# Optimization experiments

Measured on AMD Instinct MI355X. Metric: run time of the kernel, lower is better.

Reference implementation:

```python
import jax, jax.numpy as jnp
import numpy as np
import math

B, S, D = 2, 8192, 1024
NW, SHIFT = 16, 256          # num_windows, shift_window
NH, DH = 16, 64              # heads = D // dim_head
DFF = 4 * D
EPS = 1e-6


def setup_inputs() -> dict:
    key = jax.random.key(0)
    ks = jax.random.split(key, 12)
    s = 1.0 / math.sqrt(D)
    return {
        "x": jax.random.normal(ks[0], (B, S, D), jnp.float32),
        "wq": jax.random.normal(ks[1], (D, NH * DH), jnp.float32) * s,
        "wk": jax.random.normal(ks[2], (D, NH * DH), jnp.float32) * s,
        "wv": jax.random.normal(ks[3], (D, NH * DH), jnp.float32) * s,
        "wo": jax.random.normal(ks[4], (NH * DH, D), jnp.float32) * s,
        "g_attn": jnp.ones((D,), jnp.float32),
        "g_ff": jnp.ones((D,), jnp.float32),
        "w1": jax.random.normal(ks[5], (D, DFF), jnp.float32) * s,
        "b1": jnp.zeros((DFF,), jnp.float32),
        "w2": jax.random.normal(ks[6], (DFF, D), jnp.float32) * (1.0 / math.sqrt(DFF)),
        "b2": jnp.zeros((D,), jnp.float32),
    }


def _rmsnorm(x, g):
    return x * g * jax.lax.rsqrt(jnp.mean(x * x, axis=-1, keepdims=True) + EPS)


def reference(x, wq, wk, wv, wo, g_attn, g_ff, w1, b1, w2, b2):
    skip = x
    h = _rmsnorm(x, g_attn)
    # shift (note: source rolls by -shift both before AND after attention)
    h = jnp.roll(h, -SHIFT, axis=1)
    # window partition: [B, NW, n, D]
    n = S // NW
    h = h.reshape(B, NW, n, D)
    q = (h @ wq).reshape(B, NW, n, NH, DH)
    k = (h @ wk).reshape(B, NW, n, NH, DH)
    v = (h @ wv).reshape(B, NW, n, NH, DH)
    scores = jnp.einsum('bwqhd,bwkhd->bwhqk', q, k) * (1.0 / math.sqrt(DH))
    a = jax.nn.softmax(scores, axis=-1)
    o = jnp.einsum('bwhqk,bwkhd->bwqhd', a, v).reshape(B, NW, n, NH * DH)
    o = (o @ wo).reshape(B, S, D)
    o = jnp.roll(o, -SHIFT, axis=1)  # faithful to source (rolls -shift again)
    x = o + skip
    skip = x
    h = _rmsnorm(x, g_ff)
    h = jax.nn.gelu(h @ w1 + b1) @ w2 + b2
    return h + skip
```

## Files before the change

### kernel.cpp

```cpp
#include <hip/hip_runtime.h>
#include <stdint.h>

#define S_LEN 8192
#define D_DIM 1024
#define SHIFT_W 256
#define NROWS 16384

typedef __bf16 bf16;
typedef __bf16 bf16x8 __attribute__((ext_vector_type(8)));
typedef __bf16 bf16x4 __attribute__((ext_vector_type(4)));
typedef float f32x4 __attribute__((ext_vector_type(4)));

typedef __attribute__((address_space(1))) const void gas_t;
typedef __attribute__((address_space(3))) void las_t;

__device__ __forceinline__ void load_lds16(const void* g, void* l) {
  __builtin_amdgcn_global_load_lds((gas_t*)g, (las_t*)l, 16, 0, 0);
}

__device__ __forceinline__ int xcd_swizzle(int orig, int nwg) {
  return (orig & 7) * (nwg >> 3) + (orig >> 3);
}

__global__ __launch_bounds__(256) void k_transpose_cvt(const float* __restrict__ in,
                                                       bf16* __restrict__ out,
                                                       int R, int C) {
  __shared__ float tile[32][33];
  int lx = threadIdx.x & 31, ly = threadIdx.x >> 5;
  int tc = blockIdx.x * 32, tr = blockIdx.y * 32;
#pragma unroll
  for (int i = 0; i < 4; i++)
    tile[ly + i * 8][lx] = in[(size_t)(tr + ly + i * 8) * C + tc + lx];
  __syncthreads();
#pragma unroll
  for (int i = 0; i < 4; i++)
    out[(size_t)(tc + ly + i * 8) * R + tr + lx] = (bf16)tile[lx][ly + i * 8];
}

__global__ __launch_bounds__(256) void k_rmsnorm(const float* __restrict__ x,
                                                 const float* __restrict__ g,
                                                 bf16* __restrict__ out, int shift) {
  int row = blockIdx.x;
  int b = row >> 13, r = row & (S_LEN - 1);
  int src = (b << 13) | ((r + shift) & (S_LEN - 1));
  int t = threadIdx.x;
  float4 v = *(const float4*)(x + (size_t)src * D_DIM + t * 4);
  float ss = v.x * v.x + v.y * v.y + v.z * v.z + v.w * v.w;
#pragma unroll
  for (int off = 32; off; off >>= 1) ss += __shfl_xor(ss, off);
  __shared__ float red[4];
  if ((t & 63) == 0) red[t >> 6] = ss;
  __syncthreads();
  ss = red[0] + red[1] + red[2] + red[3];
  float sc = rsqrtf(ss * (1.0f / D_DIM) + 1e-6f);
  float4 gv = *(const float4*)(g + t * 4);
  bf16x4 o;
  o[0] = (bf16)(v.x * gv.x * sc);
  o[1] = (bf16)(v.y * gv.y * sc);
  o[2] = (bf16)(v.z * gv.z * sc);
  o[3] = (bf16)(v.w * gv.w * sc);
  *(bf16x4*)(out + (size_t)row * D_DIM + t * 4) = o;
}

#define VM8 asm volatile("s_waitcnt vmcnt(8)" ::: "memory")
#define VM4 asm volatile("s_waitcnt vmcnt(4)" ::: "memory")
#define VM0 asm volatile("s_waitcnt vmcnt(0)" ::: "memory")
#define BAR __builtin_amdgcn_s_barrier()

#define STAGE(kbase, kk, dbuf)                                        \
  {                                                                   \
    const bf16* _ga = gAs + (kbase) + (kk) * 32;                      \
    const bf16* _gb = gBs + (kbase) + (kk) * 32;                      \
    char* _lb = smem + (dbuf) * 65536 + (kk) * 16384 + wv * 1024;     \
    load_lds16(_ga, _lb);                                             \
    load_lds16(_ga + 128 * (size_t)K, _lb + 8192);                    \
    load_lds16(_gb, _lb + 32768);                                     \
    load_lds16(_gb + 128 * (size_t)K, _lb + 40960);                   \
  }

#define DS_A(mh, kkof)                                                \
  {                                                                   \
    _Pragma("unroll") for (int mf = 0; mf < 4; mf++)                  \
        a[mf] = *(const bf16x8*)(Ac + (kkof) + aBase + (mh) * 4096 + mf * 1024); \
  }
#define DS_B(kkof)                                                    \
  {                                                                   \
    _Pragma("unroll") for (int nf = 0; nf < 4; nf++)                  \
        bfr[nf] = *(const bf16x8*)(Ac + (kkof) + bBase + nf * 1024);  \
  }
#define MFMA16(mh)                                                    \
  {                                                                   \
    __builtin_amdgcn_s_setprio(1);                                    \
    _Pragma("unroll") for (int mf = 0; mf < 4; mf++)                  \
        _Pragma("unroll") for (int nf = 0; nf < 4; nf++)              \
            acc[(mh) * 4 + mf][nf] = __builtin_amdgcn_mfma_f32_16x16x32_bf16( \
                a[mf], bfr[nf], acc[(mh) * 4 + mf][nf], 0, 0, 0);     \
    __builtin_amdgcn_s_setprio(0);                                    \
  }

template <int EPI>
__global__ __launch_bounds__(512, 2) void k_gemm(const bf16* __restrict__ A,
                                                 const bf16* __restrict__ BT,
                                                 bf16* __restrict__ obf,
                                                 float* __restrict__ of32,
                                                 const float* __restrict__ bias,
                                                 const float* __restrict__ skip,
                                                 int K, int ldc) {
  extern __shared__ char smem[];
  const int tid = threadIdx.x;
  const int wv = tid >> 6, lane = tid & 63;
  const int lr = lane & 15, lg = lane >> 4;
  const int wm = wv >> 2, wn = wv & 3;

  const int NB = gridDim.x >> 6;
  const int xcd = blockIdx.x & 7;
  const int l = blockIdx.x >> 3;
  const int mb = ((xcd & 3) << 4) + (l & 15);
  const int nb = (xcd >> 2) * (NB >> 1) + (l >> 4);
  const int m0 = mb * 256, n0 = nb * 256;

  const int sr = ((tid >> 6) << 4) + ((tid >> 2) & 15);
  const int skoff = (((tid & 3) ^ ((tid >> 3) & 3)) << 3);
  const bf16* gAs = A + (size_t)(m0 + sr) * K + skoff;
  const bf16* gBs = BT + (size_t)(n0 + sr) * K + skoff;

  const int kchunk = (lg ^ ((lr >> 1) & 3)) << 4;
  const int aBase = wm * 8192 + lr * 64 + kchunk;
  const int bBase = 32768 + wn * 4096 + lr * 64 + kchunk;

  f32x4 acc[8][4] = {};
  const int nt = K >> 6;

  STAGE(0, 0, 0);
  STAGE(0, 1, 0);
  STAGE(64, 0, 1);
  VM8;
  BAR;

  int cur = 0;
  for (int t = 0; t < nt; ++t) {
    const int k0 = t << 6;
    const char* Ac = smem + cur * 65536;
    bf16x8 a[4], bfr[4];
    DS_A(0, 0);
    DS_B(0);
    BAR;
    if (t + 1 < nt) STAGE(k0 + 64, 1, cur ^ 1);
    MFMA16(0);
    DS_A(1, 0);
    BAR;
    MFMA16(1);
    if (t + 1 < nt) { VM8; } else { VM0; }
    BAR;
    DS_A(0, 16384);
    DS_B(16384);
    BAR;
    if (t + 2 < nt) STAGE(k0 + 128, 0, cur);
    MFMA16(0);
    DS_A(1, 16384);
    BAR;
    MFMA16(1);
    if (t + 1 < nt) {
      if (t + 2 < nt) { VM8; } else { VM4; }
      BAR;
    }
    cur ^= 1;
  }

  float* lds_f = (float*)smem;
  const int erow = tid >> 3;
  const int ecol0 = (tid & 7) * 4;
#pragma unroll
  for (int mh = 0; mh < 2; mh++)
#pragma unroll
    for (int wmr = 0; wmr < 2; wmr++) {
      BAR;
      if (wm == wmr) {
#pragma unroll
        for (int mf = 0; mf < 4; mf++) {
          int lrow = mf * 16 + lg * 4;
#pragma unroll
          for (int nf = 0; nf < 4; nf++) {
            int lcol = wn * 64 + nf * 16 + lr;
#pragma unroll
            for (int ii = 0; ii < 4; ii++)
              lds_f[(lrow + ii) * 260 + lcol] = acc[mh * 4 + mf][nf][ii];
          }
        }
      }
      BAR;
      int gr = m0 + wmr * 128 + mh * 64 + erow;
      size_t orow;
      if constexpr (EPI == 1) {
        int b = gr >> 13, rr = gr & (S_LEN - 1);
        orow = (size_t)((b << 13) | ((rr - SHIFT_W) & (S_LEN - 1))) * ldc;
      } else {
        orow = (size_t)gr * ldc;
      }
#pragma unroll
      for (int j = 0; j < 8; j++) {
        f32x4 v = *(const f32x4*)&lds_f[erow * 260 + ecol0 + j * 32];
        int col = n0 + ecol0 + j * 32;
        if constexpr (EPI == 0) {
          bf16x4 o;
#pragma unroll
          for (int e = 0; e < 4; e++) o[e] = (bf16)v[e];
          *(bf16x4*)(obf + orow + col) = o;
        } else if constexpr (EPI == 1) {
          f32x4 s = *(const f32x4*)(skip + orow + col);
          f32x4 r = v + s;
          *(f32x4*)(of32 + orow + col) = r;
        } else if constexpr (EPI == 2) {
          f32x4 bi = *(const f32x4*)(bias + col);
          bf16x4 o;
#pragma unroll
          for (int e = 0; e < 4; e++) {
            float z = v[e] + bi[e];
            float u = 0.7978845608f * (z + 0.044715f * z * z * z);
            u = fminf(fmaxf(u, -15.f), 15.f);
            float ex = __expf(2.f * u);
            o[e] = (bf16)(0.5f * z * (1.f + (ex - 1.f) / (ex + 1.f)));
          }
          *(bf16x4*)(obf + orow + col) = o;
        } else {
          f32x4 bi = *(const f32x4*)(bias + col);
          f32x4 s = *(const f32x4*)(skip + orow + col);
          f32x4 r = v + bi + s;
          *(f32x4*)(of32 + orow + col) = r;
        }
      }
    }
}

__global__ __launch_bounds__(256) void k_attn(const bf16* __restrict__ qkv,
                                              bf16* __restrict__ out) {
  __shared__ __align__(16) char Qs[8192];
  __shared__ __align__(16) char Ks[8192];
  __shared__ __align__(16) char Vs[8192];
  __shared__ __align__(16) char Ps[4][2048];
  const int tid = threadIdx.x;
  const int wave = tid >> 6, lane = tid & 63;
  const int lr = lane & 15, lg = lane >> 4;
  const int bid = xcd_swizzle(blockIdx.x, gridDim.x);
  const int qt = bid & 7;
  const int h = (bid >> 3) & 15;
  const int bw = bid >> 7;
  const int rowbase = bw * 512;
  const int qrow0 = rowbase + qt * 64;

  {
    int r = tid >> 2, c0 = tid & 3;
    const bf16* src = qkv + (size_t)(qrow0 + r) * 3072 + h * 64;
#pragma unroll
    for (int j = 0; j < 2; j++) {
      int ch = c0 + j * 4;
      uint4 val = *(const uint4*)(src + ch * 8);
      int byte = (r * 128 + ch * 16) ^ ((r & 7) << 4);
      *(uint4*)(Qs + byte) = val;
    }
  }
  __syncthreads();
  bf16x8 qf[2];
  {
    int qr = wave * 16 + lr;
#pragma unroll
    for (int kk = 0; kk < 2; kk++) {
      int byte = (qr * 128 + (kk * 32 + lg * 8) * 2) ^ ((qr & 7) << 4);
      qf[kk] = *(const bf16x8*)(Qs + byte);
    }
  }

  f32x4 oacc[4] = {};
  float m_run = -__builtin_inff(), l_run = 0.f;

  for (int kt = 0; kt < 8; ++kt) {
    __syncthreads();
    {
      int r = tid >> 2, c0 = tid & 3;
      const bf16* ksrc = qkv + (size_t)(rowbase + kt * 64 + r) * 3072 + 1024 + h * 64;
      const bf16* vsrc = ksrc + 1024;
#pragma unroll
      for (int j = 0; j < 2; j++) {
        int ch = c0 + j * 4;
        uint4 val = *(const uint4*)(ksrc + ch * 8);
        int byte = (r * 128 + ch * 16) ^ ((r & 7) << 4);
        *(uint4*)(Ks + byte) = val;
      }
#pragma unroll
      for (int j = 0; j < 2; j++) {
        int ch = c0 + j * 4;
        bf16x8 vv = *(const bf16x8*)(vsrc + ch * 8);
#pragma unroll
        for (int e = 0; e < 8; e++) {
          int d = ch * 8 + e;
          int byte = (d * 128 + r * 2) ^ ((d & 7) << 4);
          *(bf16*)(Vs + byte) = vv[e];
        }
      }
    }
    __syncthreads();
    f32x4 sc[4] = {};
#pragma unroll
    for (int kk = 0; kk < 2; kk++)
#pragma unroll
      for (int mf = 0; mf < 4; mf++) {
        int kr = mf * 16 + lr;
        int byte = (kr * 128 + (kk * 32 + lg * 8) * 2) ^ ((kr & 7) << 4);
        bf16x8 kf = *(const bf16x8*)(Ks + byte);
        sc[mf] = __builtin_amdgcn_mfma_f32_16x16x32_bf16(kf, qf[kk], sc[mf], 0, 0, 0);
      }
    float mx = -__builtin_inff();
#pragma unroll
    for (int mf = 0; mf < 4; mf++)
#pragma unroll
      for (int i = 0; i < 4; i++) mx = fmaxf(mx, sc[mf][i]);
    mx = fmaxf(mx, __shfl_xor(mx, 16));
    mx = fmaxf(mx, __shfl_xor(mx, 32));
    float mnew = fmaxf(m_run, mx);
    float alpha = __expf(0.125f * (m_run - mnew));
    float lsum = 0.f;
    float ps[4][4];
#pragma unroll
    for (int mf = 0; mf < 4; mf++)
#pragma unroll
      for (int i = 0; i < 4; i++) {
        float p = __expf(0.125f * (sc[mf][i] - mnew));
        ps[mf][i] = p;
        lsum += p;
      }
    lsum += __shfl_xor(lsum, 16);
    lsum += __shfl_xor(lsum, 32);
    l_run = l_run * alpha + lsum;
    m_run = mnew;
#pragma unroll
    for (int dm = 0; dm < 4; dm++) oacc[dm] *= alpha;
#pragma unroll
    for (int mf = 0; mf < 4; mf++) {
      bf16x4 pv;
#pragma unroll
      for (int i = 0; i < 4; i++) pv[i] = (bf16)ps[mf][i];
      int byte = (lr * 128 + (mf * 16 + lg * 4) * 2) ^ ((lr & 7) << 4);
      *(bf16x4*)(Ps[wave] + byte) = pv;
    }
#pragma unroll
    for (int kk = 0; kk < 2; kk++) {
      int pbyte = (lr * 128 + (kk * 32 + lg * 8) * 2) ^ ((lr & 7) << 4);
      bf16x8 pf = *(const bf16x8*)(Ps[wave] + pbyte);
#pragma unroll
      for (int dm = 0; dm < 4; dm++) {
        int d = dm * 16 + lr;
        int byte = (d * 128 + (kk * 32 + lg * 8) * 2) ^ ((d & 7) << 4);
        bf16x8 vf = *(const bf16x8*)(Vs + byte);
        oacc[dm] = __builtin_amdgcn_mfma_f32_16x16x32_bf16(vf, pf, oacc[dm], 0, 0, 0);
      }
    }
  }
  float inv = 1.f / l_run;
  int rowq = qrow0 + wave * 16 + lr;
#pragma unroll
  for (int dm = 0; dm < 4; dm++) {
    bf16x4 ov;
#pragma unroll
    for (int i = 0; i < 4; i++) ov[i] = (bf16)(oacc[dm][i] * inv);
    *(bf16x4*)(out + (size_t)rowq * 1024 + h * 64 + dm * 16 + lg * 4) = ov;
  }
}

extern "C" void kernel_launch(void* const* d_in, const int* in_sizes, int n_in,
                              void* d_out, int out_size, void* d_ws, size_t ws_size,
                              hipStream_t stream) {
  const float* x = (const float*)d_in[0];
  const float* wq = (const float*)d_in[1];
  const float* wk = (const float*)d_in[2];
  const float* wv = (const float*)d_in[3];
  const float* wo = (const float*)d_in[4];
  const float* ga = (const float*)d_in[5];
  const float* gf = (const float*)d_in[6];
  const float* w1 = (const float*)d_in[7];
  const float* b1 = (const float*)d_in[8];
  const float* w2 = (const float*)d_in[9];
  const float* b2 = (const float*)d_in[10];
  float* out = (float*)d_out;

  char* ws = (char*)d_ws;
  const size_t MB = 1024 * 1024;
  bf16* wqkvT = (bf16*)(ws);
  bf16* woT = (bf16*)(ws + 6 * MB);
  bf16* w1T = (bf16*)(ws + 8 * MB);
  bf16* w2T = (bf16*)(ws + 16 * MB);
  float* x1 = (float*)(ws + 24 * MB);
  bf16* hbuf = (bf16*)(ws + 88 * MB);
  bf16* qkv = (bf16*)(ws + 120 * MB);
  bf16* mid = qkv;

  (void)hipFuncSetAttribute(reinterpret_cast<const void*>(&k_gemm<0>),
                            hipFuncAttributeMaxDynamicSharedMemorySize, 131072);
  (void)hipFuncSetAttribute(reinterpret_cast<const void*>(&k_gemm<1>),
                            hipFuncAttributeMaxDynamicSharedMemorySize, 131072);
  (void)hipFuncSetAttribute(reinterpret_cast<const void*>(&k_gemm<2>),
                            hipFuncAttributeMaxDynamicSharedMemorySize, 131072);
  (void)hipFuncSetAttribute(reinterpret_cast<const void*>(&k_gemm<3>),
                            hipFuncAttributeMaxDynamicSharedMemorySize, 131072);

  k_transpose_cvt<<<dim3(32, 32), 256, 0, stream>>>(wq, wqkvT, 1024, 1024);
  k_transpose_cvt<<<dim3(32, 32), 256, 0, stream>>>(wk, wqkvT + 1024 * 1024, 1024, 1024);
  k_transpose_cvt<<<dim3(32, 32), 256, 0, stream>>>(wv, wqkvT + 2 * 1024 * 1024, 1024, 1024);
  k_transpose_cvt<<<dim3(32, 32), 256, 0, stream>>>(wo, woT, 1024, 1024);
  k_transpose_cvt<<<dim3(128, 32), 256, 0, stream>>>(w1, w1T, 1024, 4096);
  k_transpose_cvt<<<dim3(32, 128), 256, 0, stream>>>(w2, w2T, 4096, 1024);

  k_rmsnorm<<<NROWS, 256, 0, stream>>>(x, ga, hbuf, SHIFT_W);
  k_gemm<0><<<64 * 12, 512, 131072, stream>>>(hbuf, wqkvT, qkv, nullptr, nullptr, nullptr, 1024, 3072);
  k_attn<<<4096, 256, 0, stream>>>(qkv, hbuf);
  k_gemm<1><<<64 * 4, 512, 131072, stream>>>(hbuf, woT, nullptr, x1, nullptr, x, 1024, 1024);
  k_rmsnorm<<<NROWS, 256, 0, stream>>>(x1, gf, hbuf, 0);
  k_gemm<2><<<64 * 16, 512, 131072, stream>>>(hbuf, w1T, mid, nullptr, b1, nullptr, 1024, 4096);
  k_gemm<3><<<64 * 4, 512, 131072, stream>>>(mid, w2T, nullptr, out, b2, x1, 4096, 1024);
}
```

Before: 666.1 us.

## Double-buffer LDS fragment registers to overlap ds_reads with MFMA in GEMM

Restructures the GEMM main loop to use two sets of A and B register fragments, so each shared-memory fragment read for the next MFMA batch is issued before the current batch runs. The next tile's first fragments are prefetched at the end of each iteration, and the vmcnt waits and barriers are reordered. The aim is to hide LDS read latency behind matrix instructions. The cost is more vector registers, which could cause spills or lower occupancy at launch bounds of 512 threads with 2 blocks. The new wait and barrier ordering also risks a race between global-to-LDS staging and the fragment reads.

Result: no change. 659.8 us (-0.9%).

```diff
diff --git a/kernel.cpp b/kernel.cpp
--- a/kernel.cpp
+++ b/kernel.cpp
@@ -62,7 +62,6 @@
   *(bf16x4*)(out + (size_t)row * D_DIM + t * 4) = o;
 }
 
-#define VM8 asm volatile("s_waitcnt vmcnt(8)" ::: "memory")
 #define VM4 asm volatile("s_waitcnt vmcnt(4)" ::: "memory")
 #define VM0 asm volatile("s_waitcnt vmcnt(0)" ::: "memory")
 #define BAR __builtin_amdgcn_s_barrier()
@@ -78,23 +77,23 @@
     load_lds16(_gb + 128 * (size_t)K, _lb + 40960);                   \
   }
 
-#define DS_A(mh, kkof)                                                \
+#define LOAD_A(dst, mh, kkof, base)                                   \
   {                                                                   \
     _Pragma("unroll") for (int mf = 0; mf < 4; mf++)                  \
-        a[mf] = *(const bf16x8*)(Ac + (kkof) + aBase + (mh) * 4096 + mf * 1024); \
-  }
-#define DS_B(kkof)                                                    \
+        dst[mf] = *(const bf16x8*)((base) + (kkof) + aBase + (mh) * 4096 + mf * 1024); \
+  }
+#define LOAD_B(dst, kkof, base)                                       \
   {                                                                   \
     _Pragma("unroll") for (int nf = 0; nf < 4; nf++)                  \
-        bfr[nf] = *(const bf16x8*)(Ac + (kkof) + bBase + nf * 1024);  \
-  }
-#define MFMA16(mh)                                                    \
+        dst[nf] = *(const bf16x8*)((base) + (kkof) + bBase + nf * 1024); \
+  }
+#define MFMA16(mh, A_, B_)                                            \
   {                                                                   \
     __builtin_amdgcn_s_setprio(1);                                    \
     _Pragma("unroll") for (int mf = 0; mf < 4; mf++)                  \
         _Pragma("unroll") for (int nf = 0; nf < 4; nf++)              \
             acc[(mh) * 4 + mf][nf] = __builtin_amdgcn_mfma_f32_16x16x32_bf16( \
-                a[mf], bfr[nf], acc[(mh) * 4 + mf][nf], 0, 0, 0);     \
+                A_[mf], B_[nf], acc[(mh) * 4 + mf][nf], 0, 0, 0);     \
     __builtin_amdgcn_s_setprio(0);                                    \
   }
 
@@ -131,40 +130,45 @@
   f32x4 acc[8][4] = {};
   const int nt = K >> 6;
 
+  bf16x8 aX[4], aY[4], b0[4], b1[4];
+
   STAGE(0, 0, 0);
   STAGE(0, 1, 0);
-  STAGE(64, 0, 1);
-  VM8;
+  if (nt > 1) STAGE(64, 0, 1);
+  VM4;
   BAR;
-
-  int cur = 0;
+  LOAD_A(aX, 0, 0, smem);
+  LOAD_B(b0, 0, smem);
+
   for (int t = 0; t < nt; ++t) {
-    const int k0 = t << 6;
-    const char* Ac = smem + cur * 65536;
-    bf16x8 a[4], bfr[4];
-    DS_A(0, 0);
-    DS_B(0);
+    const char* Bc = smem + (size_t)((t & 1) * 65536);
+    const char* Bn = smem + (size_t)(((t + 1) & 1) * 65536);
+    LOAD_A(aY, 1, 0, Bc);
+    if (t + 1 < nt) {
+      STAGE((t + 1) << 6, 1, (t + 1) & 1);
+      VM4;
+    }
     BAR;
-    if (t + 1 < nt) STAGE(k0 + 64, 1, cur ^ 1);
-    MFMA16(0);
-    DS_A(1, 0);
+    MFMA16(0, aX, b0);
+    LOAD_A(aX, 0, 16384, Bc);
+    LOAD_B(b1, 16384, Bc);
     BAR;
-    MFMA16(1);
-    if (t + 1 < nt) { VM8; } else { VM0; }
+    MFMA16(1, aY, b0);
+    LOAD_A(aY, 1, 16384, Bc);
+    if (t + 2 < nt) {
+      STAGE((t + 2) << 6, 0, t & 1);
+      VM4;
+    } else if (t + 1 < nt) {
+      VM0;
+    }
     BAR;
-    DS_A(0, 16384);
-    DS_B(16384);
-    BAR;
-    if (t + 2 < nt) STAGE(k0 + 128, 0, cur);
-    MFMA16(0);
-    DS_A(1, 16384);
-    BAR;
-    MFMA16(1);
+    MFMA16(0, aX, b1);
     if (t + 1 < nt) {
-      if (t + 2 < nt) { VM8; } else { VM4; }
+      LOAD_A(aX, 0, 0, Bn);
+      LOAD_B(b0, 0, Bn);
       BAR;
     }
-    cur ^= 1;
+    MFMA16(1, aY, b1);
   }
 
   float* lds_f = (float*)smem;
```
